# Kernel optimization log

Hardware: AMD Instinct MI355X
Metric: run time of the kernel (lower is better)

Reference implementation:

```python
import jax, jax.numpy as jnp
import numpy as np

B, L, E, DA, R = 256, 2048, 64, 64, 32

def setup_inputs() -> dict:
    key = jax.random.key(0)
    k1, k2, k3, k4 = jax.random.split(key, 4)
    x = jax.random.normal(k1, (B, L, E), dtype=jnp.float32)
    mask = (jax.random.uniform(k2, (B, L)) > 0.2).astype(jnp.float32)
    # glorot-uniform-like init for the small attention weights
    lim1 = np.sqrt(6.0 / (DA + E)).astype(np.float32)
    lim2 = np.sqrt(6.0 / (R + DA)).astype(np.float32)
    W1 = jax.random.uniform(k3, (DA, E), minval=-lim1, maxval=lim1, dtype=jnp.float32)
    W2 = jax.random.uniform(k4, (R, DA), minval=-lim2, maxval=lim2, dtype=jnp.float32)
    return {"x": x, "mask": mask, "W1": W1, "W2": W2}

def reference(x, mask, W1, W2):
    # x: (B,L,E), mask: (B,L), W1: (DA,E), W2: (R,DA)
    xm = x * mask[:, :, None]                       # masked inputs (B,L,E)
    H = jnp.tanh(jnp.einsum('de,ble->bdl', W1, xm))  # (B,DA,L)
    Q = jnp.einsum('rd,bdl->brl', W2, H)             # (B,R,L)
    A = jnp.exp(Q) * mask[:, None, :]                # masked exp scores (B,R,L)
    A = A / jnp.sum(A, axis=2, keepdims=True)        # normalize over L
    # dropout is identity at inference
    return jnp.einsum('brl,ble->bre', A, xm)         # (B,R,E)
```

## Files before the change

### kernel.cpp

```cpp
#include <hip/hip_runtime.h>
#include <hip/hip_bf16.h>


#define B_  256
#define L_  2048
#define E_  64
#define DA_ 64
#define R_  32
#define CH_ 8
#define NS_ 2

typedef __attribute__((ext_vector_type(8))) short bf16x8;
typedef __attribute__((ext_vector_type(4))) float f32x4;

#define HS_P 36
#define XT_P 68
#define AS_P 68
#define HS_W (128 * HS_P)
#define XT_W (64 * XT_P)
#define AS_W (32 * AS_P)
#define SS_W (32 * 16)

__device__ __forceinline__ unsigned pk(float a, float b) {
    __hip_bfloat162 h = __float22bfloat162_rn(float2{a, b});
    union { __hip_bfloat162 h2; unsigned u; } cv; cv.h2 = h;
    return cv.u;
}
__device__ __forceinline__ float bflo(unsigned u) { return __uint_as_float(u << 16); }
__device__ __forceinline__ float bfhi(unsigned u) { return __uint_as_float(u & 0xFFFF0000u); }
__device__ __forceinline__ float fast_tanh(float v) {
    float e = __builtin_amdgcn_exp2f(v * 2.885390082f);
    float r = __builtin_amdgcn_rcpf(e + 1.0f);
    return fmaf(-2.0f, r, 1.0f);
}
__device__ __forceinline__ float fast_exp(float v) {
    return __builtin_amdgcn_exp2f(v * 1.442695041f);
}

__launch_bounds__(256, 3)
__global__ void selfbi_main(const float* __restrict__ x,
                            const float* __restrict__ mask,
                            const float* __restrict__ W1,
                            const float* __restrict__ W2,
                            float* __restrict__ accp,
                            float* __restrict__ ssump) {
    __shared__ __align__(16) unsigned smem[HS_W + XT_W + AS_W + SS_W];
    unsigned* hsw = smem;
    unsigned* xtw = smem + HS_W;
    unsigned* asw = xtw + XT_W;
    float*    ssp = (float*)(asw + AS_W);

    const int b    = blockIdx.x;
    const int c    = blockIdx.y;
    const int tid  = threadIdx.x;
    const int w    = tid >> 6;
    const int lane = tid & 63;
    const int g    = lane >> 4;
    const int ml   = lane & 15;
    const int p4   = tid & 31;
    const int q8   = tid >> 5;

    bf16x8 w1f[4][2], w2f[2][2];
    #pragma unroll
    for (int mt = 0; mt < 4; ++mt)
        #pragma unroll
        for (int kb = 0; kb < 2; ++kb) {
            const float* p = W1 + (16 * mt + ml) * E_ + 32 * kb + 8 * g;
            float4 a = *(const float4*)p, bb = *(const float4*)(p + 4);
            union { bf16x8 s; unsigned u[4]; } cv;
            cv.u[0] = pk(a.x, a.y); cv.u[1] = pk(a.z, a.w);
            cv.u[2] = pk(bb.x, bb.y); cv.u[3] = pk(bb.z, bb.w);
            w1f[mt][kb] = cv.s;
        }
    #pragma unroll
    for (int nt = 0; nt < 2; ++nt)
        #pragma unroll
        for (int kb = 0; kb < 2; ++kb) {
            const float* p = W2 + (16 * nt + ml) * DA_ + 32 * kb + 8 * g;
            float4 a = *(const float4*)p, bb = *(const float4*)(p + 4);
            union { bf16x8 s; unsigned u[4]; } cv;
            cv.u[0] = pk(a.x, a.y); cv.u[1] = pk(a.z, a.w);
            cv.u[2] = pk(bb.x, bb.y); cv.u[3] = pk(bb.z, bb.w);
            w2f[nt][kb] = cv.s;
        }

    f32x4 c3[2] = {f32x4{0,0,0,0}, f32x4{0,0,0,0}};
    float ssum_acc = 0.0f;

    for (int s = 0; s < NS_; ++s) {
        if (s) __syncthreads();

        const int    l0    = c * (NS_ * 128) + s * 128;
        const size_t xbase = ((size_t)b * L_ + l0) * E_;

        float xe[4][8];
        #pragma unroll
        for (int k = 0; k < 4; ++k) {
            const float* p = x + xbase + (size_t)(4 * p4 + k) * E_ + 8 * q8;
            float4 a = *(const float4*)p, bb = *(const float4*)(p + 4);
            xe[k][0] = a.x;  xe[k][1] = a.y;  xe[k][2] = a.z;  xe[k][3] = a.w;
            xe[k][4] = bb.x; xe[k][5] = bb.y; xe[k][6] = bb.z; xe[k][7] = bb.w;
        }
        float4 gb[2][2][2];
        #pragma unroll
        for (int nt = 0; nt < 2; ++nt)
            #pragma unroll
            for (int kb = 0; kb < 2; ++kb) {
                const float* p = x + xbase + (size_t)(32 * w + 16 * nt + ml) * E_
                                 + 32 * kb + 8 * g;
                gb[nt][kb][0] = *(const float4*)p;
                gb[nt][kb][1] = *(const float4*)(p + 4);
            }
        float4 mk[2];
        #pragma unroll
        for (int mt = 0; mt < 2; ++mt)
            mk[mt] = *(const float4*)(mask + b * L_ + l0 + 32 * w + 16 * mt + 4 * g);

        #pragma unroll
        for (int j = 0; j < 8; ++j) {
            uint2 u;
            u.x = pk(xe[0][j], xe[1][j]);
            u.y = pk(xe[2][j], xe[3][j]);
            *(uint2*)&xtw[(8 * q8 + j) * XT_P + 2 * p4] = u;
        }

        bf16x8 xf[2][2];
        #pragma unroll
        for (int nt = 0; nt < 2; ++nt)
            #pragma unroll
            for (int kb = 0; kb < 2; ++kb) {
                union { bf16x8 s; unsigned u[4]; } cv;
                float4 a = gb[nt][kb][0], bb = gb[nt][kb][1];
                cv.u[0] = pk(a.x, a.y); cv.u[1] = pk(a.z, a.w);
                cv.u[2] = pk(bb.x, bb.y); cv.u[3] = pk(bb.z, bb.w);
                xf[nt][kb] = cv.s;
            }
        f32x4 c1[2][4];
        #pragma unroll
        for (int nt = 0; nt < 2; ++nt)
            #pragma unroll
            for (int mt = 0; mt < 4; ++mt) c1[nt][mt] = f32x4{0,0,0,0};
        #pragma unroll
        for (int kb = 0; kb < 2; ++kb)
            #pragma unroll
            for (int nt = 0; nt < 2; ++nt)
                #pragma unroll
                for (int mt = 0; mt < 4; ++mt)
                    c1[nt][mt] = __builtin_amdgcn_mfma_f32_16x16x32_bf16(
                        w1f[mt][kb], xf[nt][kb], c1[nt][mt], 0, 0, 0);

        #pragma unroll
        for (int nt = 0; nt < 2; ++nt) {
            const int t = 32 * w + 16 * nt + ml;
            #pragma unroll
            for (int mt = 0; mt < 4; ++mt) {
                float h0 = fast_tanh(c1[nt][mt][0]);
                float h1 = fast_tanh(c1[nt][mt][1]);
                float h2 = fast_tanh(c1[nt][mt][2]);
                float h3 = fast_tanh(c1[nt][mt][3]);
                uint2 u; u.x = pk(h0, h1); u.y = pk(h2, h3);
                *(uint2*)&hsw[t * HS_P + 8 * mt + 2 * g] = u;
            }
        }

        f32x4 c2[2][2];
        #pragma unroll
        for (int mt = 0; mt < 2; ++mt)
            #pragma unroll
            for (int nt = 0; nt < 2; ++nt) c2[mt][nt] = f32x4{0,0,0,0};
        #pragma unroll
        for (int kb = 0; kb < 2; ++kb)
            #pragma unroll
            for (int mt = 0; mt < 2; ++mt) {
                bf16x8 af = *(bf16x8*)&hsw[(32 * w + 16 * mt + ml) * HS_P
                                           + 16 * kb + 4 * g];
                #pragma unroll
                for (int nt = 0; nt < 2; ++nt)
                    c2[mt][nt] = __builtin_amdgcn_mfma_f32_16x16x32_bf16(
                        af, w2f[nt][kb], c2[mt][nt], 0, 0, 0);
            }

        float part[2] = {0.f, 0.f};
        #pragma unroll
        for (int mt = 0; mt < 2; ++mt) {
            const float m0 = mk[mt].x, m1 = mk[mt].y, m2 = mk[mt].z, m3 = mk[mt].w;
            const int tw = 16 * w + 8 * mt + 2 * g;
            #pragma unroll
            for (int nt = 0; nt < 2; ++nt) {
                float a0 = fast_exp(c2[mt][nt][0]) * m0;
                float a1 = fast_exp(c2[mt][nt][1]) * m1;
                float a2 = fast_exp(c2[mt][nt][2]) * m2;
                float a3 = fast_exp(c2[mt][nt][3]) * m3;
                uint2 u; u.x = pk(a0, a1); u.y = pk(a2, a3);
                *(uint2*)&asw[(16 * nt + ml) * AS_P + tw] = u;
                part[nt] += bflo(u.x) + bfhi(u.x) + bflo(u.y) + bfhi(u.y);
            }
        }
        #pragma unroll
        for (int nt = 0; nt < 2; ++nt)
            ssp[(16 * nt + ml) * 16 + 4 * w + g] = part[nt];

        __syncthreads();

        #pragma unroll
        for (int kb = 0; kb < 4; ++kb) {
            bf16x8 bf = *(bf16x8*)&xtw[(16 * w + ml) * XT_P + 16 * kb + 4 * g];
            #pragma unroll
            for (int mt = 0; mt < 2; ++mt) {
                bf16x8 af = *(bf16x8*)&asw[(16 * mt + ml) * AS_P + 16 * kb + 4 * g];
                c3[mt] = __builtin_amdgcn_mfma_f32_16x16x32_bf16(af, bf, c3[mt], 0, 0, 0);
            }
        }

        if (tid < 32) {
            const float4* q = (const float4*)&ssp[tid * 16];
            float4 q0 = q[0], q1 = q[1], q2 = q[2], q3 = q[3];
            ssum_acc += (q0.x + q0.y + q0.z + q0.w) + (q1.x + q1.y + q1.z + q1.w)
                      + (q2.x + q2.y + q2.z + q2.w) + (q3.x + q3.y + q3.z + q3.w);
        }
    }

    const size_t obase = (size_t)(b * CH_ + c) * (R_ * E_);
    const int e = 16 * w + ml;
    #pragma unroll
    for (int mt = 0; mt < 2; ++mt)
        #pragma unroll
        for (int reg = 0; reg < 4; ++reg) {
            const int r = 16 * mt + 4 * g + reg;
            accp[obase + r * E_ + e] = c3[mt][reg];
        }
    if (tid < 32) ssump[(b * CH_ + c) * R_ + tid] = ssum_acc;
}

__launch_bounds__(256, 4)
__global__ void selfbi_reduce(const float* __restrict__ accp,
                              const float* __restrict__ ssump,
                              float* __restrict__ out) {
    const int of = blockIdx.x * 256 + threadIdx.x;
    const int b  = of >> 11;
    const int o  = of & 2047;
    const int r  = o >> 6;
    float num = 0.f, den = 0.f;
    #pragma unroll
    for (int cc = 0; cc < CH_; ++cc) {
        num += accp[((size_t)(b * CH_ + cc)) * (R_ * E_) + o];
        den += ssump[(b * CH_ + cc) * R_ + r];
    }
    out[of] = num / den;
}

extern "C" void kernel_launch(void* const* d_in, const int* in_sizes, int n_in,
                              void* d_out, int out_size, void* d_ws, size_t ws_size,
                              hipStream_t stream) {
    const float* x    = (const float*)d_in[0];
    const float* mask = (const float*)d_in[1];
    const float* W1   = (const float*)d_in[2];
    const float* W2   = (const float*)d_in[3];
    float* out        = (float*)d_out;

    float* accp  = (float*)d_ws;
    float* ssump = accp + (size_t)B_ * CH_ * R_ * E_;

    selfbi_main<<<dim3(B_, CH_), dim3(256), 0, stream>>>(x, mask, W1, W2, accp, ssump);
    selfbi_reduce<<<dim3((B_ * R_ * E_) / 256), dim3(256), 0, stream>>>(accp, ssump, out);
}
```

Measured before the change: 227.0 us.

## Shrink per-step token tile to 64 and derive transposed x from MFMA loads

The step tile drops from 128 to 64 tokens, with four steps per block instead of two. This shrinks LDS buffers and raises the occupancy hint from 3 to 5 blocks per CU. The transposed bf16 copy of x is now written from the same registers used as MFMA operands, using XOR-swizzled 16-bit stores. That removes the second, uncoalesced global read of each x tile. Per-row exp sums are reduced with wave shuffles and combined once at the end instead of every step through shared memory. The cost is more barrier rounds per token, plus scattered 16-bit LDS stores that may conflict.

```diff
diff --git a/kernel.cpp b/kernel.cpp
--- a/kernel.cpp
+++ b/kernel.cpp
@@ -8,18 +8,18 @@
 #define DA_ 64
 #define R_  32
 #define CH_ 8
-#define NS_ 2
+#define NS_ 4
+#define TL_ 64
 
 typedef __attribute__((ext_vector_type(8))) short bf16x8;
 typedef __attribute__((ext_vector_type(4))) float f32x4;
 
 #define HS_P 36
-#define XT_P 68
-#define AS_P 68
-#define HS_W (128 * HS_P)
+#define XT_P 36
+#define AS_P 36
+#define HS_W (64 * HS_P)
 #define XT_W (64 * XT_P)
 #define AS_W (32 * AS_P)
-#define SS_W (32 * 16)
 
 __device__ __forceinline__ unsigned pk(float a, float b) {
     __hip_bfloat162 h = __float22bfloat162_rn(float2{a, b});
@@ -37,18 +37,18 @@
     return __builtin_amdgcn_exp2f(v * 1.442695041f);
 }
 
-__launch_bounds__(256, 3)
+__launch_bounds__(256, 5)
 __global__ void selfbi_main(const float* __restrict__ x,
                             const float* __restrict__ mask,
                             const float* __restrict__ W1,
                             const float* __restrict__ W2,
                             float* __restrict__ accp,
                             float* __restrict__ ssump) {
-    __shared__ __align__(16) unsigned smem[HS_W + XT_W + AS_W + SS_W];
+    __shared__ __align__(16) unsigned smem[HS_W + XT_W + AS_W + 128];
     unsigned* hsw = smem;
     unsigned* xtw = smem + HS_W;
     unsigned* asw = xtw + XT_W;
-    float*    ssp = (float*)(asw + AS_W);
+    float*    ssl = (float*)(asw + AS_W);
 
     const int b    = blockIdx.x;
     const int c    = blockIdx.y;
@@ -57,8 +57,6 @@
     const int lane = tid & 63;
     const int g    = lane >> 4;
     const int ml   = lane & 15;
-    const int p4   = tid & 31;
-    const int q8   = tid >> 5;
 
     bf16x8 w1f[4][2], w2f[2][2];
     #pragma unroll
@@ -85,138 +83,112 @@
         }
 
     f32x4 c3[2] = {f32x4{0,0,0,0}, f32x4{0,0,0,0}};
-    float ssum_acc = 0.0f;
+    float sswav0 = 0.0f, sswav1 = 0.0f;
+
+    const int trow = 16 * w + ml;
+    const int thalf = trow >> 1, tbyte = trow & 1;
 
     for (int s = 0; s < NS_; ++s) {
         if (s) __syncthreads();
 
-        const int    l0    = c * (NS_ * 128) + s * 128;
+        const int    l0    = c * (NS_ * TL_) + s * TL_;
         const size_t xbase = ((size_t)b * L_ + l0) * E_;
 
-        float xe[4][8];
-        #pragma unroll
-        for (int k = 0; k < 4; ++k) {
-            const float* p = x + xbase + (size_t)(4 * p4 + k) * E_ + 8 * q8;
-            float4 a = *(const float4*)p, bb = *(const float4*)(p + 4);
-            xe[k][0] = a.x;  xe[k][1] = a.y;  xe[k][2] = a.z;  xe[k][3] = a.w;
-            xe[k][4] = bb.x; xe[k][5] = bb.y; xe[k][6] = bb.z; xe[k][7] = bb.w;
-        }
-        float4 gb[2][2][2];
-        #pragma unroll
-        for (int nt = 0; nt < 2; ++nt)
+        const float* xr = x + xbase + (size_t)trow * E_;
+        float4 gx[2][2];
+        gx[0][0] = *(const float4*)(xr + 8 * g);
+        gx[0][1] = *(const float4*)(xr + 8 * g + 4);
+        gx[1][0] = *(const float4*)(xr + 32 + 8 * g);
+        gx[1][1] = *(const float4*)(xr + 32 + 8 * g + 4);
+        float4 mk = *(const float4*)(mask + b * L_ + l0 + 16 * w + 4 * g);
+
+        bf16x8 xf[2];
+        union { bf16x8 s; unsigned u[4]; } xc[2];
+        #pragma unroll
+        for (int kb = 0; kb < 2; ++kb) {
+            xc[kb].u[0] = pk(gx[kb][0].x, gx[kb][0].y);
+            xc[kb].u[1] = pk(gx[kb][0].z, gx[kb][0].w);
+            xc[kb].u[2] = pk(gx[kb][1].x, gx[kb][1].y);
+            xc[kb].u[3] = pk(gx[kb][1].z, gx[kb][1].w);
+            xf[kb] = xc[kb].s;
+        }
+
+        #pragma unroll
+        for (int kb = 0; kb < 2; ++kb)
+            #pragma unroll
+            for (int i = 0; i < 4; ++i) {
+                const int e0 = 32 * kb + 8 * g + 2 * i;
+                const int wd = thalf ^ (8 * g);
+                ((unsigned short*)&xtw[e0 * XT_P + wd])[tbyte] =
+                    (unsigned short)(xc[kb].u[i] & 0xFFFF);
+                ((unsigned short*)&xtw[(e0 + 1) * XT_P + wd])[tbyte] =
+                    (unsigned short)(xc[kb].u[i] >> 16);
+            }
+
+        f32x4 c1[4] = {f32x4{0,0,0,0}, f32x4{0,0,0,0}, f32x4{0,0,0,0}, f32x4{0,0,0,0}};
+        #pragma unroll
+        for (int kb = 0; kb < 2; ++kb)
+            #pragma unroll
+            for (int mt = 0; mt < 4; ++mt)
+                c1[mt] = __builtin_amdgcn_mfma_f32_16x16x32_bf16(
+                    w1f[mt][kb], xf[kb], c1[mt], 0, 0, 0);
+
+        #pragma unroll
+        for (int mt = 0; mt < 4; ++mt) {
+            float h0 = fast_tanh(c1[mt][0]);
+            float h1 = fast_tanh(c1[mt][1]);
+            float h2 = fast_tanh(c1[mt][2]);
+            float h3 = fast_tanh(c1[mt][3]);
+            uint2 u; u.x = pk(h0, h1); u.y = pk(h2, h3);
+            *(uint2*)&hsw[trow * HS_P + 8 * mt + 2 * g] = u;
+        }
+
+        f32x4 c2[2] = {f32x4{0,0,0,0}, f32x4{0,0,0,0}};
+        #pragma unroll
+        for (int kb = 0; kb < 2; ++kb) {
+            bf16x8 af = *(bf16x8*)&hsw[trow * HS_P + 16 * kb + 4 * g];
+            #pragma unroll
+            for (int nt = 0; nt < 2; ++nt)
+                c2[nt] = __builtin_amdgcn_mfma_f32_16x16x32_bf16(
+                    af, w2f[nt][kb], c2[nt], 0, 0, 0);
+        }
+
+        float part0, part1;
+        {
+            const int tw = 8 * w + 2 * g;
+            float a0 = fast_exp(c2[0][0]) * mk.x;
+            float a1 = fast_exp(c2[0][1]) * mk.y;
+            float a2 = fast_exp(c2[0][2]) * mk.z;
+            float a3 = fast_exp(c2[0][3]) * mk.w;
+            uint2 u; u.x = pk(a0, a1); u.y = pk(a2, a3);
+            *(uint2*)&asw[ml * AS_P + tw] = u;
+            part0 = bflo(u.x) + bfhi(u.x) + bflo(u.y) + bfhi(u.y);
+            a0 = fast_exp(c2[1][0]) * mk.x;
+            a1 = fast_exp(c2[1][1]) * mk.y;
+            a2 = fast_exp(c2[1][2]) * mk.z;
+            a3 = fast_exp(c2[1][3]) * mk.w;
+            u.x = pk(a0, a1); u.y = pk(a2, a3);
+            *(uint2*)&asw[(16 + ml) * AS_P + tw] = u;
+            part1 = bflo(u.x) + bfhi(u.x) + bflo(u.y) + bfhi(u.y);
+        }
+        part0 += __shfl_xor(part0, 16); part0 += __shfl_xor(part0, 32);
+        part1 += __shfl_xor(part1, 16); part1 += __shfl_xor(part1, 32);
+        sswav0 += part0; sswav1 += part1;
+
+        __syncthreads();
+
+        {
+            const int erow = 16 * w + ml;
+            const int esw  = 8 * ((erow >> 3) & 3);
             #pragma unroll
             for (int kb = 0; kb < 2; ++kb) {
-                const float* p = x + xbase + (size_t)(32 * w + 16 * nt + ml) * E_
-                                 + 32 * kb + 8 * g;
-                gb[nt][kb][0] = *(const float4*)p;
-                gb[nt][kb][1] = *(const float4*)(p + 4);
+                bf16x8 bf = *(bf16x8*)&xtw[erow * XT_P + ((16 * kb + 4 * g) ^ esw)];
+                #pragma unroll
+                for (int mt = 0; mt < 2; ++mt) {
+                    bf16x8 af = *(bf16x8*)&asw[(16 * mt + ml) * AS_P + 16 * kb + 4 * g];
+                    c3[mt] = __builtin_amdgcn_mfma_f32_16x16x32_bf16(af, bf, c3[mt], 0, 0, 0);
+                }
             }
-        float4 mk[2];
-        #pragma unroll
-        for (int mt = 0; mt < 2; ++mt)
-            mk[mt] = *(const float4*)(mask + b * L_ + l0 + 32 * w + 16 * mt + 4 * g);
-
-        #pragma unroll
-        for (int j = 0; j < 8; ++j) {
-            uint2 u;
-            u.x = pk(xe[0][j], xe[1][j]);
-            u.y = pk(xe[2][j], xe[3][j]);
-            *(uint2*)&xtw[(8 * q8 + j) * XT_P + 2 * p4] = u;
-        }
-
-        bf16x8 xf[2][2];
-        #pragma unroll
-        for (int nt = 0; nt < 2; ++nt)
-            #pragma unroll
-            for (int kb = 0; kb < 2; ++kb) {
-                union { bf16x8 s; unsigned u[4]; } cv;
-                float4 a = gb[nt][kb][0], bb = gb[nt][kb][1];
-                cv.u[0] = pk(a.x, a.y); cv.u[1] = pk(a.z, a.w);
-                cv.u[2] = pk(bb.x, bb.y); cv.u[3] = pk(bb.z, bb.w);
-                xf[nt][kb] = cv.s;
-            }
-        f32x4 c1[2][4];
-        #pragma unroll
-        for (int nt = 0; nt < 2; ++nt)
-            #pragma unroll
-            for (int mt = 0; mt < 4; ++mt) c1[nt][mt] = f32x4{0,0,0,0};
-        #pragma unroll
-        for (int kb = 0; kb < 2; ++kb)
-            #pragma unroll
-            for (int nt = 0; nt < 2; ++nt)
-                #pragma unroll
-                for (int mt = 0; mt < 4; ++mt)
-                    c1[nt][mt] = __builtin_amdgcn_mfma_f32_16x16x32_bf16(
-                        w1f[mt][kb], xf[nt][kb], c1[nt][mt], 0, 0, 0);
-
-        #pragma unroll
-        for (int nt = 0; nt < 2; ++nt) {
-            const int t = 32 * w + 16 * nt + ml;
-            #pragma unroll
-            for (int mt = 0; mt < 4; ++mt) {
-                float h0 = fast_tanh(c1[nt][mt][0]);
-                float h1 = fast_tanh(c1[nt][mt][1]);
-                float h2 = fast_tanh(c1[nt][mt][2]);
-                float h3 = fast_tanh(c1[nt][mt][3]);
-                uint2 u; u.x = pk(h0, h1); u.y = pk(h2, h3);
-                *(uint2*)&hsw[t * HS_P + 8 * mt + 2 * g] = u;
-            }
-        }
-
-        f32x4 c2[2][2];
-        #pragma unroll
-        for (int mt = 0; mt < 2; ++mt)
-            #pragma unroll
-            for (int nt = 0; nt < 2; ++nt) c2[mt][nt] = f32x4{0,0,0,0};
-        #pragma unroll
-        for (int kb = 0; kb < 2; ++kb)
-            #pragma unroll
-            for (int mt = 0; mt < 2; ++mt) {
-                bf16x8 af = *(bf16x8*)&hsw[(32 * w + 16 * mt + ml) * HS_P
-                                           + 16 * kb + 4 * g];
-                #pragma unroll
-                for (int nt = 0; nt < 2; ++nt)
-                    c2[mt][nt] = __builtin_amdgcn_mfma_f32_16x16x32_bf16(
-                        af, w2f[nt][kb], c2[mt][nt], 0, 0, 0);
-            }
-
-        float part[2] = {0.f, 0.f};
-        #pragma unroll
-        for (int mt = 0; mt < 2; ++mt) {
-            const float m0 = mk[mt].x, m1 = mk[mt].y, m2 = mk[mt].z, m3 = mk[mt].w;
-            const int tw = 16 * w + 8 * mt + 2 * g;
-            #pragma unroll
-            for (int nt = 0; nt < 2; ++nt) {
-                float a0 = fast_exp(c2[mt][nt][0]) * m0;
-                float a1 = fast_exp(c2[mt][nt][1]) * m1;
-                float a2 = fast_exp(c2[mt][nt][2]) * m2;
-                float a3 = fast_exp(c2[mt][nt][3]) * m3;
-                uint2 u; u.x = pk(a0, a1); u.y = pk(a2, a3);
-                *(uint2*)&asw[(16 * nt + ml) * AS_P + tw] = u;
-                part[nt] += bflo(u.x) + bfhi(u.x) + bflo(u.y) + bfhi(u.y);
-            }
-        }
-        #pragma unroll
-        for (int nt = 0; nt < 2; ++nt)
-            ssp[(16 * nt + ml) * 16 + 4 * w + g] = part[nt];
-
-        __syncthreads();
-
-        #pragma unroll
-        for (int kb = 0; kb < 4; ++kb) {
-            bf16x8 bf = *(bf16x8*)&xtw[(16 * w + ml) * XT_P + 16 * kb + 4 * g];
-            #pragma unroll
-            for (int mt = 0; mt < 2; ++mt) {
-                bf16x8 af = *(bf16x8*)&asw[(16 * mt + ml) * AS_P + 16 * kb + 4 * g];
-                c3[mt] = __builtin_amdgcn_mfma_f32_16x16x32_bf16(af, bf, c3[mt], 0, 0, 0);
-            }
-        }
-
-        if (tid < 32) {
-            const float4* q = (const float4*)&ssp[tid * 16];
-            float4 q0 = q[0], q1 = q[1], q2 = q[2], q3 = q[3];
-            ssum_acc += (q0.x + q0.y + q0.z + q0.w) + (q1.x + q1.y + q1.z + q1.w)
-                      + (q2.x + q2.y + q2.z + q2.w) + (q3.x + q3.y + q3.z + q3.w);
         }
     }
 
@@ -229,7 +201,14 @@
             const int r = 16 * mt + 4 * g + reg;
             accp[obase + r * E_ + e] = c3[mt][reg];
         }
-    if (tid < 32) ssump[(b * CH_ + c) * R_ + tid] = ssum_acc;
+    if (g == 0) {
+        ssl[w * 32 + ml]      = sswav0;
+        ssl[w * 32 + 16 + ml] = sswav1;
+    }
+    __syncthreads();
+    if (tid < 32)
+        ssump[(b * CH_ + c) * R_ + tid] =
+            ssl[tid] + ssl[32 + tid] + ssl[64 + tid] + ssl[96 + tid];
 }
 
 __launch_bounds__(256, 4)
```

After: 248.3 us. 9.4% more time.
